# Kernel optimization log

Hardware: AMD Instinct MI355X
Metric: run time of the kernel (lower is better)

Reference implementation:

```python
import jax, jax.numpy as jnp
import numpy as np

# ---- constants from FlyingCartpole.__init__ defaults ----
MASS_Q = 2.0
MASS_P = 0.1
MASS = MASS_Q + MASS_P              # total mass m
JMAT = jnp.array([[0.0023, 0.0, 0.0], [0.0, 0.0023, 0.0], [0.0, 0.0, 0.004]], jnp.float32)
JINV = jnp.linalg.inv(JMAT)
L = 0.5                              # pendulum length
GVEC = jnp.array([0.0, 0.0, -9.81], jnp.float32)
MOTOR_DIST = 0.175
KF = 1.0
KM = 0.025
DT = 0.05
ACT_SCALE = 10.0
U_HOVER = -MASS * (-9.81) / ACT_SCALE / KF / 4.0   # per-motor hover throttle
_SS = np.array([[1.0, 1, 0], [1.0, -1, 0], [-1.0, -1, 0], [-1.0, 1, 0]], np.float32)
SS = jnp.asarray(_SS / np.linalg.norm(_SS, axis=-1, keepdims=True))  # [4,3] unit arms


def mrp2quat(m):
    # q = [1 - |m|^2, 2m] / (1 + |m|^2)
    n2 = jnp.sum(m * m, axis=-1, keepdims=True)
    return jnp.concatenate([1.0 - n2, 2.0 * m], axis=-1) / (1.0 + n2)


def quatrot(q, v):
    # rotate vector v by unit quaternion q = [s, qv]
    s, qv = q[..., :1], q[..., 1:]
    return v + 2.0 * jnp.cross(qv, jnp.cross(qv, v) + s * v)


def w2pdotkinematics_mrp(m, w):
    # mdot = 1/4 [(1-|m|^2) I + 2 [m]_x + 2 m m^T] w
    n2 = jnp.sum(m * m, axis=-1, keepdims=True)
    mw = jnp.sum(m * w, axis=-1, keepdims=True)
    return 0.25 * ((1.0 - n2) * w + 2.0 * jnp.cross(m, w) + 2.0 * m * mw)


def dynamics_(x, u):
    # state: [r(3), m(3), theta(1), v(3), w(3), theta_dot(1)]
    u = ACT_SCALE * (u + U_HOVER)
    m = x[..., 3:6]
    v = x[..., 7:10]
    w = x[..., 10:13]
    theta = x[..., 6:7]
    theta_dot = x[..., 13:14]

    q = mrp2quat(m)

    # forces (body frame): thrust + gravity rotated by q(-m)
    Fz = KF * jnp.sum(u, axis=-1)                     # [B]
    z = jnp.zeros_like(Fz)
    Fvec = jnp.stack([z, z, Fz], axis=-1)             # [B,3]
    f = Fvec + quatrot(mrp2quat(-m), MASS * GVEC)     # [B,3]

    # moments
    tau3 = KM * (u[..., 0] - u[..., 1] + u[..., 2] - u[..., 3])
    tau = jnp.stack([z, z, tau3], axis=-1)            # [B,3]
    zu = jnp.zeros_like(u)
    thrust = jnp.stack([zu, zu, KF * u], axis=-1)     # [B,4,3]
    tau = tau + jnp.cross(MOTOR_DIST * SS, thrust).sum(axis=-2)

    mdot = w2pdotkinematics_mrp(m, w)
    pdot = quatrot(q, v)
    vdot = f / MASS - jnp.cross(w, v)
    Jw = jnp.einsum('ij,bj->bi', JMAT, w)
    wdot = jnp.einsum('ij,bj->bi', JINV, tau - jnp.cross(w, Jw))

    x_ddot = quatrot(q, vdot)[..., 0:1]
    theta_ddot = (GVEC[2] * jnp.sin(theta) + x_ddot * jnp.cos(theta)) / L
    return jnp.concatenate([pdot, mdot, theta_dot, vdot, wdot, theta_ddot], axis=-1)


def rk4_dynamics(x, u):
    dt, dt2 = DT, DT / 2.0
    k1 = dynamics_(x, u)
    k2 = dynamics_(x + dt2 * k1, u)
    k3 = dynamics_(x + dt2 * k2, u)
    k4 = dynamics_(x + dt * k3, u)
    return x + dt / 6.0 * (k1 + 2.0 * k2 + 2.0 * k3 + k4)


def setup_inputs() -> dict:
    key = jax.random.key(0)
    kx, ku = jax.random.split(key)
    B = 2097152
    x = jax.random.normal(kx, (B, 14), dtype=jnp.float32)
    u = jax.random.normal(ku, (B, 4), dtype=jnp.float32)
    return {"x": x, "u": u}


def reference(x, u):
    return rk4_dynamics(x, u)
```

## Files before the change

kernel.cpp:

```cpp
#include <hip/hip_runtime.h>
#include <math.h>

namespace fc {

typedef float vf2 __attribute__((ext_vector_type(2)));
typedef float vf4 __attribute__((ext_vector_type(4)));

__device__ __forceinline__ vf2 sp(float c) { return vf2{c, c}; }

constexpr float ACT_SCALE = 10.0f;
constexpr float U_HOVER   = 0.515025f;
constexpr float INV_MASS  = 1.0f / 2.1f;
constexpr float KM        = 0.025f;
constexpr float TAUC      = 0.175f * 0.70710678f;
constexpr float JXY       = 0.0023f;
constexpr float JZ        = 0.004f;
constexpr float INV_JXY   = 1.0f / 0.0023f;
constexpr float INV_JZ    = 1.0f / 0.004f;
constexpr float G3        = -9.81f;
constexpr float INV_L     = 2.0f;
constexpr float DT        = 0.05f;
constexpr float DT2       = 0.05f * 0.5f;
constexpr float DT6       = 0.05f / 6.0f;

__device__ __forceinline__ void dyn2(const vf2* xt, vf2 FzM,
                                     vf2 taux, vf2 tauy, vf2 tauz, vf2* dx) {
  vf2 mx = xt[3], my = xt[4], mz = xt[5], th = xt[6];
  vf2 vx = xt[7], vy = xt[8], vz = xt[9];
  vf2 wx = xt[10], wy = xt[11], wz = xt[12];

  vf2 n2 = mx * mx + my * my + mz * mz;
  vf2 inv;
  inv.x = __builtin_amdgcn_rcpf(1.0f + n2.x);
  inv.y = __builtin_amdgcn_rcpf(1.0f + n2.y);
  vf2 s  = (sp(1.0f) - n2) * inv;
  vf2 qx = sp(2.0f) * mx * inv;
  vf2 qy = sp(2.0f) * my * inv;
  vf2 qz = sp(2.0f) * mz * inv;

  vf2 gtx = qy * sp(-G3);
  vf2 gty = qx * sp(G3);
  vf2 gtz = s * sp(G3);
  vf2 gx = sp(-2.0f) * (qy * gtz - qz * gty);
  vf2 gy = sp(-2.0f) * (qz * gtx - qx * gtz);
  vf2 gz = sp(G3) + sp(-2.0f) * (qx * gty - qy * gtx);

  vf2 tx = qy * vz - qz * vy + s * vx;
  vf2 ty = qz * vx - qx * vz + s * vy;
  vf2 tz = qx * vy - qy * vx + s * vz;
  dx[0] = vx + sp(2.0f) * (qy * tz - qz * ty);
  dx[1] = vy + sp(2.0f) * (qz * tx - qx * tz);
  dx[2] = vz + sp(2.0f) * (qx * ty - qy * tx);

  vf2 mw  = mx * wx + my * wy + mz * wz;
  vf2 on2 = sp(1.0f) - n2;
  dx[3] = sp(0.25f) * (on2 * wx + sp(2.0f) * (my * wz - mz * wy) + sp(2.0f) * mx * mw);
  dx[4] = sp(0.25f) * (on2 * wy + sp(2.0f) * (mz * wx - mx * wz) + sp(2.0f) * my * mw);
  dx[5] = sp(0.25f) * (on2 * wz + sp(2.0f) * (mx * wy - my * wx) + sp(2.0f) * mz * mw);

  dx[6] = xt[13];

  vf2 vdx = gx - (wy * vz - wz * vy);
  vf2 vdy = gy - (wz * vx - wx * vz);
  vf2 vdz = FzM + gz - (wx * vy - wy * vx);
  dx[7] = vdx; dx[8] = vdy; dx[9] = vdz;

  vf2 Jwx = sp(JXY) * wx, Jwy = sp(JXY) * wy, Jwz = sp(JZ) * wz;
  dx[10] = (taux - (wy * Jwz - wz * Jwy)) * sp(INV_JXY);
  dx[11] = (tauy - (wz * Jwx - wx * Jwz)) * sp(INV_JXY);
  dx[12] = (tauz - (wx * Jwy - wy * Jwx)) * sp(INV_JZ);

  vf2 t2y = qz * vdx - qx * vdz + s * vdy;
  vf2 t2z = qx * vdy - qy * vdx + s * vdz;
  vf2 rx  = vdx + sp(2.0f) * (qy * t2z - qz * t2y);
  vf2 st, ct;
  st.x = __sinf(th.x); st.y = __sinf(th.y);
  ct.x = __cosf(th.x); ct.y = __cosf(th.y);
  dx[13] = (sp(G3) * st + rx * ct) * sp(INV_L);
}

__device__ __forceinline__ void rk4_rows2(const vf2* x0, vf4 uA, vf4 uB, vf2* o) {
  vf2 su0 = sp(ACT_SCALE) * (vf2{uA.x, uB.x} + sp(U_HOVER));
  vf2 su1 = sp(ACT_SCALE) * (vf2{uA.y, uB.y} + sp(U_HOVER));
  vf2 su2 = sp(ACT_SCALE) * (vf2{uA.z, uB.z} + sp(U_HOVER));
  vf2 su3 = sp(ACT_SCALE) * (vf2{uA.w, uB.w} + sp(U_HOVER));

  vf2 Fz   = ((su0 + su1) + su2) + su3;
  vf2 FzM  = Fz * sp(INV_MASS);
  vf2 tauz = sp(KM) * (((su0 - su1) + su2) - su3);
  vf2 taux = ((sp(TAUC) * su0 + sp(-TAUC) * su1) + sp(-TAUC) * su2) + sp(TAUC) * su3;
  vf2 tauy = ((sp(-TAUC) * su0 + sp(-TAUC) * su1) + sp(TAUC) * su2) + sp(TAUC) * su3;

  vf2 xt[14], kk[14], acc[14];
  dyn2(x0, FzM, taux, tauy, tauz, kk);
  #pragma unroll
  for (int j = 0; j < 14; ++j) { acc[j] = kk[j]; xt[j] = x0[j] + sp(DT2) * kk[j]; }
  dyn2(xt, FzM, taux, tauy, tauz, kk);
  #pragma unroll
  for (int j = 0; j < 14; ++j) { acc[j] += sp(2.0f) * kk[j]; xt[j] = x0[j] + sp(DT2) * kk[j]; }
  dyn2(xt, FzM, taux, tauy, tauz, kk);
  #pragma unroll
  for (int j = 0; j < 14; ++j) { acc[j] += sp(2.0f) * kk[j]; xt[j] = x0[j] + sp(DT) * kk[j]; }
  dyn2(xt, FzM, taux, tauy, tauz, kk);
  #pragma unroll
  for (int j = 0; j < 14; ++j) o[j] = x0[j] + sp(DT6) * (acc[j] + kk[j]);
}

__global__ __launch_bounds__(256) void fc_rk4_kernel(const float* __restrict__ x,
                                                     const float* __restrict__ u,
                                                     float* __restrict__ out,
                                                     int n) {
  __shared__ float xs[512 * 14];
  const int t = threadIdx.x;
  const long long base = (long long)blockIdx.x * 512;

  if (base + 512 <= (long long)n) {
    const vf4* xg4 = (const vf4*)(x + base * 14);
    vf4* xs4 = (vf4*)xs;
    #pragma unroll
    for (int k = 0; k < 7; ++k)
      xs4[t + k * 256] = __builtin_nontemporal_load(xg4 + t + k * 256);
    __syncthreads();

    vf4* mine = (vf4*)(xs + t * 28);
    vf4 a0 = mine[0], a1 = mine[1], a2 = mine[2], a3 = mine[3],
        a4 = mine[4], a5 = mine[5], a6 = mine[6];

    vf2 x0[14] = {
      {a0.x, a3.z}, {a0.y, a3.w}, {a0.z, a4.x}, {a0.w, a4.y},
      {a1.x, a4.z}, {a1.y, a4.w}, {a1.z, a5.x}, {a1.w, a5.y},
      {a2.x, a5.z}, {a2.y, a5.w}, {a2.z, a6.x}, {a2.w, a6.y},
      {a3.x, a6.z}, {a3.y, a6.w}};

    const vf4* ug = (const vf4*)(u + base * 4) + 2 * t;
    vf4 uA = ug[0];
    vf4 uB = ug[1];

    vf2 o[14];
    rk4_rows2(x0, uA, uB, o);

    mine[0] = vf4{o[0].x,  o[1].x,  o[2].x,  o[3].x};
    mine[1] = vf4{o[4].x,  o[5].x,  o[6].x,  o[7].x};
    mine[2] = vf4{o[8].x,  o[9].x,  o[10].x, o[11].x};
    mine[3] = vf4{o[12].x, o[13].x, o[0].y,  o[1].y};
    mine[4] = vf4{o[2].y,  o[3].y,  o[4].y,  o[5].y};
    mine[5] = vf4{o[6].y,  o[7].y,  o[8].y,  o[9].y};
    mine[6] = vf4{o[10].y, o[11].y, o[12].y, o[13].y};
    __syncthreads();

    vf4* og4 = (vf4*)(out + base * 14);
    #pragma unroll
    for (int k = 0; k < 7; ++k)
      __builtin_nontemporal_store(xs4[t + k * 256], og4 + t + k * 256);
  } else {
    #pragma unroll
    for (int k = 0; k < 2; ++k) {
      long long r = base + 2LL * t + k;
      if (r < n) {
        vf2 x0[14];
        #pragma unroll
        for (int j = 0; j < 14; ++j) { float v = x[r * 14 + j]; x0[j] = vf2{v, v}; }
        vf4 uv = *(const vf4*)(u + r * 4);
        vf2 o[14];
        rk4_rows2(x0, uv, uv, o);
        #pragma unroll
        for (int j = 0; j < 14; ++j) out[r * 14 + j] = o[j].x;
      }
    }
  }
}

}

extern "C" void kernel_launch(void* const* d_in, const int* in_sizes, int n_in,
                              void* d_out, int out_size, void* d_ws, size_t ws_size,
                              hipStream_t stream) {
  const float* x = (const float*)d_in[0];
  const float* u = (const float*)d_in[1];
  float* out = (float*)d_out;
  const int n = in_sizes[0] / 14;
  const int grid = (n + 511) / 512;
  hipLaunchKernelGGL(fc::fc_rk4_kernel, dim3(grid), dim3(256), 0, stream,
                     x, u, out, n);
}
```

Measured before the change: 50.19 us.

## Use persistent grid-stride blocks with register prefetch of the next tile

Replaces one-block-per-tile launch with a persistent grid of at most 1024 blocks that loop over tiles with a grid stride. The next tile's x and u are loaded into registers while the current tile is computed, to overlap global loads with the RK4 arithmetic. The tail rows are handled by block 0. This raises register pressure (extra vf4 prefetch registers), which may lower occupancy, and fewer blocks may leave less latency hiding through parallelism.

```diff
diff --git a/kernel.cpp b/kernel.cpp
--- a/kernel.cpp
+++ b/kernel.cpp
@@ -109,62 +109,105 @@
 __global__ __launch_bounds__(256) void fc_rk4_kernel(const float* __restrict__ x,
                                                      const float* __restrict__ u,
                                                      float* __restrict__ out,
-                                                     int n) {
+                                                     int n, int nfull) {
   __shared__ float xs[512 * 14];
   const int t = threadIdx.x;
-  const long long base = (long long)blockIdx.x * 512;
-
-  if (base + 512 <= (long long)n) {
-    const vf4* xg4 = (const vf4*)(x + base * 14);
-    vf4* xs4 = (vf4*)xs;
-    #pragma unroll
-    for (int k = 0; k < 7; ++k)
-      xs4[t + k * 256] = __builtin_nontemporal_load(xg4 + t + k * 256);
-    __syncthreads();
-
-    vf4* mine = (vf4*)(xs + t * 28);
-    vf4 a0 = mine[0], a1 = mine[1], a2 = mine[2], a3 = mine[3],
-        a4 = mine[4], a5 = mine[5], a6 = mine[6];
-
-    vf2 x0[14] = {
-      {a0.x, a3.z}, {a0.y, a3.w}, {a0.z, a4.x}, {a0.w, a4.y},
-      {a1.x, a4.z}, {a1.y, a4.w}, {a1.z, a5.x}, {a1.w, a5.y},
-      {a2.x, a5.z}, {a2.y, a5.w}, {a2.z, a6.x}, {a2.w, a6.y},
-      {a3.x, a6.z}, {a3.y, a6.w}};
-
-    const vf4* ug = (const vf4*)(u + base * 4) + 2 * t;
-    vf4 uA = ug[0];
-    vf4 uB = ug[1];
-
-    vf2 o[14];
-    rk4_rows2(x0, uA, uB, o);
-
-    mine[0] = vf4{o[0].x,  o[1].x,  o[2].x,  o[3].x};
-    mine[1] = vf4{o[4].x,  o[5].x,  o[6].x,  o[7].x};
-    mine[2] = vf4{o[8].x,  o[9].x,  o[10].x, o[11].x};
-    mine[3] = vf4{o[12].x, o[13].x, o[0].y,  o[1].y};
-    mine[4] = vf4{o[2].y,  o[3].y,  o[4].y,  o[5].y};
-    mine[5] = vf4{o[6].y,  o[7].y,  o[8].y,  o[9].y};
-    mine[6] = vf4{o[10].y, o[11].y, o[12].y, o[13].y};
-    __syncthreads();
-
-    vf4* og4 = (vf4*)(out + base * 14);
-    #pragma unroll
-    for (int k = 0; k < 7; ++k)
-      __builtin_nontemporal_store(xs4[t + k * 256], og4 + t + k * 256);
-  } else {
+  const int stride = gridDim.x;
+  int tile = blockIdx.x;
+
+  if (tile < nfull) {
+    vf4 r0, r1, r2, r3, r4, r5, r6, uA, uB;
+    {
+      const vf4* xg4 = (const vf4*)(x + (long long)tile * 512 * 14);
+      r0 = __builtin_nontemporal_load(xg4 + t);
+      r1 = __builtin_nontemporal_load(xg4 + t + 256);
+      r2 = __builtin_nontemporal_load(xg4 + t + 512);
+      r3 = __builtin_nontemporal_load(xg4 + t + 768);
+      r4 = __builtin_nontemporal_load(xg4 + t + 1024);
+      r5 = __builtin_nontemporal_load(xg4 + t + 1280);
+      r6 = __builtin_nontemporal_load(xg4 + t + 1536);
+      const vf4* ug = (const vf4*)(u + (long long)tile * 512 * 4) + 2 * t;
+      uA = ug[0]; uB = ug[1];
+    }
+    while (true) {
+      vf4* xs4 = (vf4*)xs;
+      xs4[t]        = r0;
+      xs4[t + 256]  = r1;
+      xs4[t + 512]  = r2;
+      xs4[t + 768]  = r3;
+      xs4[t + 1024] = r4;
+      xs4[t + 1280] = r5;
+      xs4[t + 1536] = r6;
+      __syncthreads();
+
+      const int next = tile + stride;
+      const bool have_next = next < nfull;
+      vf4 p0, p1, p2, p3, p4, p5, p6, uAn, uBn;
+      if (have_next) {
+        const vf4* xg4 = (const vf4*)(x + (long long)next * 512 * 14);
+        p0 = __builtin_nontemporal_load(xg4 + t);
+        p1 = __builtin_nontemporal_load(xg4 + t + 256);
+        p2 = __builtin_nontemporal_load(xg4 + t + 512);
+        p3 = __builtin_nontemporal_load(xg4 + t + 768);
+        p4 = __builtin_nontemporal_load(xg4 + t + 1024);
+        p5 = __builtin_nontemporal_load(xg4 + t + 1280);
+        p6 = __builtin_nontemporal_load(xg4 + t + 1536);
+        const vf4* ug = (const vf4*)(u + (long long)next * 512 * 4) + 2 * t;
+        uAn = ug[0]; uBn = ug[1];
+      }
+
+      vf4* mine = (vf4*)(xs + t * 28);
+      vf4 a0 = mine[0], a1 = mine[1], a2 = mine[2], a3 = mine[3],
+          a4 = mine[4], a5 = mine[5], a6 = mine[6];
+      vf2 x0[14] = {
+        {a0.x, a3.z}, {a0.y, a3.w}, {a0.z, a4.x}, {a0.w, a4.y},
+        {a1.x, a4.z}, {a1.y, a4.w}, {a1.z, a5.x}, {a1.w, a5.y},
+        {a2.x, a5.z}, {a2.y, a5.w}, {a2.z, a6.x}, {a2.w, a6.y},
+        {a3.x, a6.z}, {a3.y, a6.w}};
+
+      vf2 o[14];
+      rk4_rows2(x0, uA, uB, o);
+
+      mine[0] = vf4{o[0].x,  o[1].x,  o[2].x,  o[3].x};
+      mine[1] = vf4{o[4].x,  o[5].x,  o[6].x,  o[7].x};
+      mine[2] = vf4{o[8].x,  o[9].x,  o[10].x, o[11].x};
+      mine[3] = vf4{o[12].x, o[13].x, o[0].y,  o[1].y};
+      mine[4] = vf4{o[2].y,  o[3].y,  o[4].y,  o[5].y};
+      mine[5] = vf4{o[6].y,  o[7].y,  o[8].y,  o[9].y};
+      mine[6] = vf4{o[10].y, o[11].y, o[12].y, o[13].y};
+      __syncthreads();
+
+      vf4* og4 = (vf4*)(out + (long long)tile * 512 * 14);
+      __builtin_nontemporal_store(xs4[t],        og4 + t);
+      __builtin_nontemporal_store(xs4[t + 256],  og4 + t + 256);
+      __builtin_nontemporal_store(xs4[t + 512],  og4 + t + 512);
+      __builtin_nontemporal_store(xs4[t + 768],  og4 + t + 768);
+      __builtin_nontemporal_store(xs4[t + 1024], og4 + t + 1024);
+      __builtin_nontemporal_store(xs4[t + 1280], og4 + t + 1280);
+      __builtin_nontemporal_store(xs4[t + 1536], og4 + t + 1536);
+
+      if (!have_next) break;
+      tile = next;
+      r0 = p0; r1 = p1; r2 = p2; r3 = p3; r4 = p4; r5 = p5; r6 = p6;
+      uA = uAn; uB = uBn;
+      __syncthreads();
+    }
+  }
+
+  const long long tbase = (long long)nfull * 512;
+  if (blockIdx.x == 0 && tbase < n) {
     #pragma unroll
     for (int k = 0; k < 2; ++k) {
-      long long r = base + 2LL * t + k;
-      if (r < n) {
+      long long rrow = tbase + 2LL * t + k;
+      if (rrow < n) {
         vf2 x0[14];
         #pragma unroll
-        for (int j = 0; j < 14; ++j) { float v = x[r * 14 + j]; x0[j] = vf2{v, v}; }
-        vf4 uv = *(const vf4*)(u + r * 4);
+        for (int j = 0; j < 14; ++j) { float v = x[rrow * 14 + j]; x0[j] = vf2{v, v}; }
+        vf4 uv = *(const vf4*)(u + rrow * 4);
         vf2 o[14];
         rk4_rows2(x0, uv, uv, o);
         #pragma unroll
-        for (int j = 0; j < 14; ++j) out[r * 14 + j] = o[j].x;
+        for (int j = 0; j < 14; ++j) out[rrow * 14 + j] = o[j].x;
       }
     }
   }
@@ -179,7 +222,8 @@
   const float* u = (const float*)d_in[1];
   float* out = (float*)d_out;
   const int n = in_sizes[0] / 14;
-  const int grid = (n + 511) / 512;
+  const int nfull = n / 512;
+  int grid = nfull < 1024 ? (nfull > 0 ? nfull : 1) : 1024;
   hipLaunchKernelGGL(fc::fc_rk4_kernel, dim3(grid), dim3(256), 0, stream,
-                     x, u, out, n);
-}
+                     x, u, out, n, nfull);
+}
```

Measured after the change: 52.71 us. 1.05x slower.

## Use per-wave direct global-to-LDS loads and drop block barriers

Applied to the files above, without the earlier changes.

Each wavefront now handles its own 128-row slice of shared memory, filled with global_load_lds async copies that go straight into LDS instead of through registers. Because no wave touches another wave's slice, the two block-wide __syncthreads are replaced by per-wave s_waitcnt waits, and the u loads are issued before the wait so they overlap the copy. This cuts register traffic and barrier stalls, but relies on intra-wave LDS ordering and drops the nontemporal hint on the input loads.

```diff
diff --git a/kernel.cpp b/kernel.cpp
--- a/kernel.cpp
+++ b/kernel.cpp
@@ -112,29 +112,38 @@
                                                      int n) {
   __shared__ float xs[512 * 14];
   const int t = threadIdx.x;
+  const int lane = t & 63;
+  const int w = t >> 6;
   const long long base = (long long)blockIdx.x * 512;
 
   if (base + 512 <= (long long)n) {
-    const vf4* xg4 = (const vf4*)(x + base * 14);
-    vf4* xs4 = (vf4*)xs;
+    const long long wrow = base + w * 128;
+    float* ws = xs + w * 1792;
+
+    typedef __attribute__((address_space(3))) float lds_f;
+    typedef const __attribute__((address_space(1))) float gbl_f;
+    gbl_f* gsrc = (gbl_f*)(x + wrow * 14);
+    lds_f* ldst = (lds_f*)ws;
     #pragma unroll
     for (int k = 0; k < 7; ++k)
-      xs4[t + k * 256] = __builtin_nontemporal_load(xg4 + t + k * 256);
-    __syncthreads();
+      __builtin_amdgcn_global_load_lds(
+          (const __attribute__((address_space(1))) void*)(gsrc + k * 256 + lane * 4),
+          (__attribute__((address_space(3))) void*)(ldst + k * 256), 16, 0, 0);
 
-    vf4* mine = (vf4*)(xs + t * 28);
+    const vf4* ug = (const vf4*)(u + wrow * 4);
+    vf4 uA = ug[2 * lane];
+    vf4 uB = ug[2 * lane + 1];
+
+    asm volatile("s_waitcnt vmcnt(0)" ::: "memory");
+
+    vf4* mine = (vf4*)(ws + lane * 28);
     vf4 a0 = mine[0], a1 = mine[1], a2 = mine[2], a3 = mine[3],
         a4 = mine[4], a5 = mine[5], a6 = mine[6];
-
     vf2 x0[14] = {
       {a0.x, a3.z}, {a0.y, a3.w}, {a0.z, a4.x}, {a0.w, a4.y},
       {a1.x, a4.z}, {a1.y, a4.w}, {a1.z, a5.x}, {a1.w, a5.y},
       {a2.x, a5.z}, {a2.y, a5.w}, {a2.z, a6.x}, {a2.w, a6.y},
       {a3.x, a6.z}, {a3.y, a6.w}};
-
-    const vf4* ug = (const vf4*)(u + base * 4) + 2 * t;
-    vf4 uA = ug[0];
-    vf4 uB = ug[1];
 
     vf2 o[14];
     rk4_rows2(x0, uA, uB, o);
@@ -146,12 +155,13 @@
     mine[4] = vf4{o[2].y,  o[3].y,  o[4].y,  o[5].y};
     mine[5] = vf4{o[6].y,  o[7].y,  o[8].y,  o[9].y};
     mine[6] = vf4{o[10].y, o[11].y, o[12].y, o[13].y};
-    __syncthreads();
+    asm volatile("s_waitcnt lgkmcnt(0)" ::: "memory");
 
-    vf4* og4 = (vf4*)(out + base * 14);
+    const vf4* ws4 = (const vf4*)ws;
+    vf4* og4 = (vf4*)(out + wrow * 14);
     #pragma unroll
     for (int k = 0; k < 7; ++k)
-      __builtin_nontemporal_store(xs4[t + k * 256], og4 + t + k * 256);
+      __builtin_nontemporal_store(ws4[k * 64 + lane], og4 + k * 64 + lane);
   } else {
     #pragma unroll
     for (int k = 0; k < 2; ++k) {
```

Measured after the change: 45.55 us. 1.1x faster.
